# Kernel tuning notes

Measured on AMD Instinct MI355X. Metric: run time of the kernel, lower is better.

## Reference

```python
import jax, jax.numpy as jnp
import numpy as np

N_NODES = 100000
N_EDGES = 1200000
N_GRAPHS = 100  # hardcoded batch_size=100 in the original module


def gcn_conv(x, src, dst, W, b, n):
    """PyG GCNConv: x' = D^{-1/2} (A+I) D^{-1/2} (x W) + b, with self-loops appended."""
    x = x @ W  # [n, out]
    loop = jnp.arange(n, dtype=src.dtype)
    s = jnp.concatenate([src, loop])
    d = jnp.concatenate([dst, loop])
    deg = jax.ops.segment_sum(jnp.ones_like(d, dtype=x.dtype), d, num_segments=n)
    dinv = jax.lax.rsqrt(deg)  # deg >= 1 because of self-loops
    norm = dinv[s] * dinv[d]  # [E+n]
    out = jax.ops.segment_sum(x[s] * norm[:, None], d, num_segments=n)
    return out + b


def setup_inputs() -> dict:
    key = jax.random.key(0)
    ks = jax.random.split(key, 20)
    x = jax.random.normal(ks[0], (N_NODES, 5), dtype=jnp.float32)
    edge_index = jax.random.randint(ks[1], (2, N_EDGES), 0, N_NODES, dtype=jnp.int64)
    batch = jnp.sort(jax.random.randint(ks[2], (N_NODES,), 0, N_GRAPHS, dtype=jnp.int64))

    def lin(k, i, o):
        kw, kb = jax.random.split(k)
        W = jax.random.normal(kw, (i, o), dtype=jnp.float32) * (1.0 / np.sqrt(i))
        b = jax.random.normal(kb, (o,), dtype=jnp.float32) * 0.01
        return W, b

    W1, b1 = lin(ks[3], 5, 32)
    W2, b2 = lin(ks[4], 32, 64)
    nn1_W, nn1_b = lin(ks[5], 64, 124)
    nn2_W, nn2_b = lin(ks[6], 124 * 4, 64)
    W4, b4 = lin(ks[7], 64, 32)
    nn3_W, nn3_b = lin(ks[8], 32, 16)
    nn4_W, nn4_b = lin(ks[9], 16, 1)
    return {
        "x": x, "edge_index": edge_index, "batch": batch,
        "W1": W1, "b1": b1, "W2": W2, "b2": b2,
        "nn1_W": nn1_W, "nn1_b": nn1_b, "nn2_W": nn2_W, "nn2_b": nn2_b,
        "W4": W4, "b4": b4, "nn3_W": nn3_W, "nn3_b": nn3_b,
        "nn4_W": nn4_W, "nn4_b": nn4_b,
    }


def reference(x, edge_index, batch, W1, b1, W2, b2, nn1_W, nn1_b, nn2_W, nn2_b,
              W4, b4, nn3_W, nn3_b, nn4_W, nn4_b):
    src, dst = edge_index[0], edge_index[1]
    h = jax.nn.relu(gcn_conv(x, src, dst, W1, b1, N_NODES))
    h = jax.nn.relu(gcn_conv(h, src, dst, W2, b2, N_NODES))
    h = h @ nn1_W + nn1_b  # [N, 124]

    # four-way scatter pooling over graph ids
    cnt = jax.ops.segment_sum(jnp.ones((N_NODES,), h.dtype), batch, num_segments=N_GRAPHS)
    nonempty = (cnt > 0)[:, None]
    a = jax.ops.segment_max(h, batch, num_segments=N_GRAPHS)
    a = jnp.where(nonempty, a, 0.0)
    b_ = jax.ops.segment_min(h, batch, num_segments=N_GRAPHS)
    b_ = jnp.where(nonempty, b_, 0.0)
    c = jax.ops.segment_sum(h, batch, num_segments=N_GRAPHS)
    d = c / jnp.maximum(cnt, 1.0)[:, None]

    g = jax.nn.relu(jnp.concatenate([a, b_, c, d], axis=1))  # [100, 496]
    g = g @ nn2_W + nn2_b  # [100, 64]

    # conv4 over self-loop-only edge_index on the 100 pooled graph nodes
    loop = jnp.arange(N_GRAPHS)
    g = jax.nn.relu(gcn_conv(g, loop, loop, W4, b4, N_GRAPHS))
    g = jax.nn.relu(g @ nn3_W + nn3_b)
    return g @ nn4_W + nn4_b  # [100, 1]
```

## Files before the change

### kernel.cpp

```cpp
#include <hip/hip_runtime.h>
#include <hip/hip_bf16.h>
#include <math.h>

#define N_NODES  100000
#define N_EDGES  1200000
#define N_GRAPHS 100
#define SCAN_B   1024
#define XRNG     ((N_NODES + 7) / 8)
#define PARTS    16

__global__ void k_degslot(const int* __restrict__ dst, int* __restrict__ deg,
                          int* __restrict__ slotpos, int e) {
    int i = blockIdx.x * blockDim.x + threadIdx.x;
    if (i < e) slotpos[i] = atomicAdd(&deg[dst[i]], 1);
}

__global__ __launch_bounds__(256) void k_fill_x(
    const int* __restrict__ src, const int* __restrict__ dst,
    const int* __restrict__ slotpos, const int* __restrict__ row_ptr,
    int* __restrict__ csr_src, int e, int nchunk) {
    int r = blockIdx.x & 7;
    int chunk = blockIdx.x >> 3;
    int lo = r * XRNG;
    int per = (e + nchunk - 1) / nchunk;
    int beg = chunk * per;
    int end = beg + per < e ? beg + per : e;
    for (int i = beg + threadIdx.x; i < end; i += 256) {
        int d = dst[i];
        if ((unsigned)(d - lo) < (unsigned)XRNG)
            csr_src[row_ptr[d] + slotpos[i]] = src[i];
    }
}

__global__ void k_block_sums(const int* __restrict__ deg, int* __restrict__ bsum, int n) {
    int i = blockIdx.x * SCAN_B + threadIdx.x;
    int v = (i < n) ? deg[i] : 0;
    #pragma unroll
    for (int d = 32; d > 0; d >>= 1) v += __shfl_xor(v, d);
    __shared__ int wsum[SCAN_B / 64];
    int lane = threadIdx.x & 63, w = threadIdx.x >> 6;
    if (lane == 0) wsum[w] = v;
    __syncthreads();
    if (threadIdx.x == 0) {
        int s = 0;
        #pragma unroll
        for (int k = 0; k < SCAN_B / 64; k++) s += wsum[k];
        bsum[blockIdx.x] = s;
    }
}

__global__ void k_scan_bsums(int* __restrict__ bsum, int nb) {
    __shared__ int s[256];
    int t = threadIdx.x;
    int v = (t < nb) ? bsum[t] : 0;
    s[t] = v;
    __syncthreads();
    for (int d = 1; d < 256; d <<= 1) {
        int u = (t >= d) ? s[t - d] : 0;
        __syncthreads();
        s[t] += u;
        __syncthreads();
    }
    if (t < nb) bsum[t] = s[t] - v;
}

__global__ void k_scan_final(const int* __restrict__ deg, const int* __restrict__ bsum,
                             const float* __restrict__ x,
                             int* __restrict__ row_ptr, float* __restrict__ dinv,
                             float* __restrict__ y0, int n, int n_edges) {
    int b = blockIdx.x;
    int i = b * SCAN_B + threadIdx.x;
    int v = (i < n) ? deg[i] : 0;
    int lane = threadIdx.x & 63, w = threadIdx.x >> 6;
    int inc = v;
    #pragma unroll
    for (int d = 1; d < 64; d <<= 1) {
        int u = __shfl_up(inc, d);
        if (lane >= d) inc += u;
    }
    __shared__ int wsum[SCAN_B / 64];
    __shared__ int woff[SCAN_B / 64];
    if (lane == 63) wsum[w] = inc;
    __syncthreads();
    if (threadIdx.x == 0) {
        int s = 0;
        #pragma unroll
        for (int k = 0; k < SCAN_B / 64; k++) { woff[k] = s; s += wsum[k]; }
    }
    __syncthreads();
    int excl = bsum[b] + woff[w] + (inc - v);
    if (i < n) {
        row_ptr[i] = excl;
        float di = rsqrtf((float)(v + 1));
        dinv[i] = di;
        float4 q0, q1;
        q0.x = x[i * 5 + 0] * di;
        q0.y = x[i * 5 + 1] * di;
        q0.z = x[i * 5 + 2] * di;
        q0.w = x[i * 5 + 3] * di;
        q1.x = x[i * 5 + 4] * di;
        q1.y = 0.f; q1.z = 0.f; q1.w = 0.f;
        *(float4*)&y0[(size_t)i * 8]     = q0;
        *(float4*)&y0[(size_t)i * 8 + 4] = q1;
    }
    if (b == 0 && threadIdx.x == 0) row_ptr[n] = n_edges;
}

__global__ __launch_bounds__(256) void k_agg1(
    const int* __restrict__ row_ptr, const int* __restrict__ csr_src,
    const float* __restrict__ y0, const float* __restrict__ dinv,
    const float* __restrict__ W1, const float* __restrict__ b1,
    float* __restrict__ y1, int n) {
    int wave = (blockIdx.x * blockDim.x + threadIdx.x) >> 6;
    if (wave >= n) return;
    int lane = threadIdx.x & 63;
    int f = lane & 7, ec = lane >> 3;
    int start = row_ptr[wave], end = row_ptr[wave + 1];
    float acc = 0.f;
    for (int e = start + ec; e < end; e += 8) {
        int s = csr_src[e];
        acc += y0[(size_t)s * 8 + f];
    }
    if (ec == 0) acc += y0[(size_t)wave * 8 + f];
    acc += __shfl_down(acc, 32);
    acc += __shfl_down(acc, 16);
    acc += __shfl_down(acc, 8);
    float di = dinv[wave];
    float s0[5];
    #pragma unroll
    for (int k = 0; k < 5; k++) s0[k] = __shfl(acc, k) * di;
    int fo = lane & 31;
    float hv = b1[fo];
    #pragma unroll
    for (int k = 0; k < 5; k++) hv += s0[k] * W1[k * 32 + fo];
    hv = hv > 0.f ? hv : 0.f;
    if (lane < 32) y1[(size_t)wave * 32 + lane] = hv * di;
}

__global__ __launch_bounds__(256) void k_agg2g(
    const int* __restrict__ row_ptr, const int* __restrict__ csr_src,
    const float* __restrict__ y1, const float* __restrict__ dinv,
    float* __restrict__ sv, int n) {
    int wave = (blockIdx.x * blockDim.x + threadIdx.x) >> 6;
    if (wave >= n) return;
    int lane = threadIdx.x & 63;
    int ec = lane >> 3, fq = lane & 7;
    int start = row_ptr[wave], end = row_ptr[wave + 1];
    float4 a0 = make_float4(0.f, 0.f, 0.f, 0.f);
    float4 a1 = make_float4(0.f, 0.f, 0.f, 0.f);
    int e = start + ec;
    for (; e + 8 < end; e += 16) {
        int s0 = csr_src[e], s1 = csr_src[e + 8];
        float4 v0 = *(const float4*)&y1[(size_t)s0 * 32 + fq * 4];
        float4 v1 = *(const float4*)&y1[(size_t)s1 * 32 + fq * 4];
        a0.x += v0.x; a0.y += v0.y; a0.z += v0.z; a0.w += v0.w;
        a1.x += v1.x; a1.y += v1.y; a1.z += v1.z; a1.w += v1.w;
    }
    for (; e < end; e += 8) {
        int s0 = csr_src[e];
        float4 v0 = *(const float4*)&y1[(size_t)s0 * 32 + fq * 4];
        a0.x += v0.x; a0.y += v0.y; a0.z += v0.z; a0.w += v0.w;
    }
    a0.x += a1.x; a0.y += a1.y; a0.z += a1.z; a0.w += a1.w;
    if (ec == 0) {
        float4 sl = *(const float4*)&y1[(size_t)wave * 32 + fq * 4];
        a0.x += sl.x; a0.y += sl.y; a0.z += sl.z; a0.w += sl.w;
    }
    a0.x += __shfl_down(a0.x, 32); a0.y += __shfl_down(a0.y, 32);
    a0.z += __shfl_down(a0.z, 32); a0.w += __shfl_down(a0.w, 32);
    a0.x += __shfl_down(a0.x, 16); a0.y += __shfl_down(a0.y, 16);
    a0.z += __shfl_down(a0.z, 16); a0.w += __shfl_down(a0.w, 16);
    a0.x += __shfl_down(a0.x, 8);  a0.y += __shfl_down(a0.y, 8);
    a0.z += __shfl_down(a0.z, 8);  a0.w += __shfl_down(a0.w, 8);
    if (lane < 8) {
        float di = dinv[wave];
        float4 r;
        r.x = a0.x * di; r.y = a0.y * di; r.z = a0.z * di; r.w = a0.w * di;
        *(float4*)&sv[(size_t)wave * 32 + fq * 4] = r;
    }
}

#define LTS 68
__global__ __launch_bounds__(256) void k_l2mm(
    const float* __restrict__ sv, const float* __restrict__ W2,
    const float* __restrict__ b2, const float* __restrict__ nn1W,
    const float* __restrict__ nn1b, float* __restrict__ h, int n) {
    __shared__ float lsW2[32 * 64];
    __shared__ float lsN[64 * 128];
    __shared__ float lsT[64 * LTS];

    int tid = threadIdx.x;
    int nb = blockIdx.x * 64;

    #pragma unroll
    for (int i = 0; i < 8; i++) lsW2[tid + i * 256] = W2[tid + i * 256];
    for (int idx = tid; idx < 64 * 124; idx += 256)
        lsN[(idx / 124) * 128 + (idx % 124)] = nn1W[idx];
    if (tid < 256) lsN[(tid >> 2) * 128 + 124 + (tid & 3)] = 0.f;
    {
        int node = tid >> 2, kq = (tid & 3) * 8;
        float4 v0, v1;
        if (nb + node < n) {
            v0 = *(const float4*)&sv[(size_t)(nb + node) * 32 + kq];
            v1 = *(const float4*)&sv[(size_t)(nb + node) * 32 + kq + 4];
        } else {
            v0 = make_float4(0.f, 0.f, 0.f, 0.f); v1 = v0;
        }
        lsT[(kq + 0) * LTS + node] = v0.x;
        lsT[(kq + 1) * LTS + node] = v0.y;
        lsT[(kq + 2) * LTS + node] = v0.z;
        lsT[(kq + 3) * LTS + node] = v0.w;
        lsT[(kq + 4) * LTS + node] = v1.x;
        lsT[(kq + 5) * LTS + node] = v1.y;
        lsT[(kq + 6) * LTS + node] = v1.z;
        lsT[(kq + 7) * LTS + node] = v1.w;
    }
    __syncthreads();

    int tf = tid & 15;
    int tn = tid >> 4;

    float c1[4][4] = {};
    #pragma unroll 4
    for (int k = 0; k < 32; k++) {
        float4 a = *(const float4*)&lsT[k * LTS + tn * 4];
        float4 w = *(const float4*)&lsW2[k * 64 + tf * 4];
        const float av[4] = {a.x, a.y, a.z, a.w};
        const float wv[4] = {w.x, w.y, w.z, w.w};
        #pragma unroll
        for (int i = 0; i < 4; i++)
            #pragma unroll
            for (int j = 0; j < 4; j++) c1[i][j] += av[i] * wv[j];
    }
    __syncthreads();
    {
        float4 bb = *(const float4*)&b2[tf * 4];
        const float bv[4] = {bb.x, bb.y, bb.z, bb.w};
        #pragma unroll
        for (int j = 0; j < 4; j++) {
            float4 col;
            col.x = fmaxf(c1[0][j] + bv[j], 0.f);
            col.y = fmaxf(c1[1][j] + bv[j], 0.f);
            col.z = fmaxf(c1[2][j] + bv[j], 0.f);
            col.w = fmaxf(c1[3][j] + bv[j], 0.f);
            *(float4*)&lsT[(tf * 4 + j) * LTS + tn * 4] = col;
        }
    }
    __syncthreads();

    float c2a[4][4] = {}, c2b[4][4] = {};
    #pragma unroll 2
    for (int k = 0; k < 64; k++) {
        float4 a  = *(const float4*)&lsT[k * LTS + tn * 4];
        float4 w1 = *(const float4*)&lsN[k * 128 + tf * 4];
        float4 w2 = *(const float4*)&lsN[k * 128 + 64 + tf * 4];
        const float av[4] = {a.x, a.y, a.z, a.w};
        const float w1v[4] = {w1.x, w1.y, w1.z, w1.w};
        const float w2v[4] = {w2.x, w2.y, w2.z, w2.w};
        #pragma unroll
        for (int i = 0; i < 4; i++)
            #pragma unroll
            for (int j = 0; j < 4; j++) {
                c2a[i][j] += av[i] * w1v[j];
                c2b[i][j] += av[i] * w2v[j];
            }
    }
    {
        float4 ba = *(const float4*)&nn1b[tf * 4];
        const float bav[4] = {ba.x, ba.y, ba.z, ba.w};
        float bbv[4] = {0.f, 0.f, 0.f, 0.f};
        if (tf < 15) {
            float4 bb = *(const float4*)&nn1b[64 + tf * 4];
            bbv[0] = bb.x; bbv[1] = bb.y; bbv[2] = bb.z; bbv[3] = bb.w;
        }
        #pragma unroll
        for (int i = 0; i < 4; i++) {
            int node = nb + tn * 4 + i;
            if (node >= n) break;
            float4 oa, ob;
            oa.x = c2a[i][0] + bav[0]; oa.y = c2a[i][1] + bav[1];
            oa.z = c2a[i][2] + bav[2]; oa.w = c2a[i][3] + bav[3];
            *(float4*)&h[(size_t)node * 124 + tf * 4] = oa;
            if (tf < 15) {
                ob.x = c2b[i][0] + bbv[0]; ob.y = c2b[i][1] + bbv[1];
                ob.z = c2b[i][2] + bbv[2]; ob.w = c2b[i][3] + bbv[3];
                *(float4*)&h[(size_t)node * 124 + 64 + tf * 4] = ob;
            }
        }
    }
}

__global__ __launch_bounds__(512) void k_pool_a(
    const float* __restrict__ h, const int* __restrict__ batch,
    float* __restrict__ pmax, float* __restrict__ pmin, float* __restrict__ psum,
    int n) {
    int g = blockIdx.x / PARTS, r = blockIdx.x % PARTS;
    __shared__ int sb[2];
    if (threadIdx.x < 2) {
        int target = g + threadIdx.x;
        int lo = 0, hi = n;
        while (lo < hi) {
            int mid = (lo + hi) >> 1;
            if (batch[mid] < target) lo = mid + 1; else hi = mid;
        }
        sb[threadIdx.x] = lo;
    }
    __syncthreads();
    int start = sb[0], end = sb[1];
    int t = threadIdx.x;
    int f = t & 127, r2 = t >> 7;
    float vmax = -INFINITY, vmin = INFINITY, vsum = 0.f;
    if (f < 124) {
        for (int node = start + r * 4 + r2; node < end; node += PARTS * 4) {
            float v = h[(size_t)node * 124 + f];
            vmax = fmaxf(vmax, v);
            vmin = fminf(vmin, v);
            vsum += v;
        }
    }
    __shared__ float smax[4][128], smin[4][128], ssum[4][128];
    smax[r2][f] = vmax; smin[r2][f] = vmin; ssum[r2][f] = vsum;
    __syncthreads();
    if (r2 == 0) {
        #pragma unroll
        for (int k = 1; k < 4; k++) {
            vmax = fmaxf(vmax, smax[k][f]);
            vmin = fminf(vmin, smin[k][f]);
            vsum += ssum[k][f];
        }
        int idx = (g * PARTS + r) * 128 + f;
        pmax[idx] = vmax; pmin[idx] = vmin; psum[idx] = vsum;
    }
}

__global__ __launch_bounds__(256) void k_head(
    const float* __restrict__ pmax, const float* __restrict__ pmin,
    const float* __restrict__ psum, const int* __restrict__ batch,
    const float* __restrict__ nn2W, const float* __restrict__ nn2b,
    const float* __restrict__ W4,   const float* __restrict__ b4,
    const float* __restrict__ nn3W, const float* __restrict__ nn3b,
    const float* __restrict__ nn4W, const float* __restrict__ nn4b,
    float* __restrict__ out, int n) {
    int g = blockIdx.x, tid = threadIdx.x;
    int lane = tid & 63, w = tid >> 6;
    __shared__ float lg[496];
    __shared__ float part[4][64];
    __shared__ int sb[2];
    if (tid < 2) {
        int target = g + tid;
        int lo = 0, hi = n;
        while (lo < hi) {
            int mid = (lo + hi) >> 1;
            if (batch[mid] < target) lo = mid + 1; else hi = mid;
        }
        sb[tid] = lo;
    }
    __syncthreads();
    if (tid < 124) {
        float vmax = -INFINITY, vmin = INFINITY, vsum = 0.f;
        #pragma unroll 4
        for (int r = 0; r < PARTS; r++) {
            int idx = (g * PARTS + r) * 128 + tid;
            vmax = fmaxf(vmax, pmax[idx]);
            vmin = fminf(vmin, pmin[idx]);
            vsum += psum[idx];
        }
        int cnt = sb[1] - sb[0];
        float a = (cnt > 0) ? vmax : 0.f;
        float b = (cnt > 0) ? vmin : 0.f;
        lg[tid]       = fmaxf(a, 0.f);
        lg[124 + tid] = fmaxf(b, 0.f);
        lg[248 + tid] = fmaxf(vsum, 0.f);
        lg[372 + tid] = fmaxf(vsum / fmaxf((float)cnt, 1.f), 0.f);
    }
    __syncthreads();
    float acc = 0.f;
    int k0 = w * 124;
    #pragma unroll 4
    for (int k = k0; k < k0 + 124; k++)
        acc += lg[k] * nn2W[k * 64 + lane];
    part[w][lane] = acc;
    __syncthreads();
    if (w == 0) {
        float g1 = part[0][lane] + part[1][lane] + part[2][lane] + part[3][lane]
                 + nn2b[lane];
        float acc2 = (lane < 32) ? b4[lane] : 0.f;
        #pragma unroll 8
        for (int k = 0; k < 64; k++) {
            float v = __shfl(g1, k);
            if (lane < 32) acc2 += v * W4[k * 32 + lane];
        }
        float g2 = fmaxf(acc2, 0.f);
        float acc3 = (lane < 16) ? nn3b[lane] : 0.f;
        #pragma unroll 8
        for (int k = 0; k < 32; k++) {
            float v = __shfl(g2, k);
            if (lane < 16) acc3 += v * nn3W[k * 16 + lane];
        }
        float g3 = fmaxf(acc3, 0.f);
        float p = (lane < 16) ? g3 * nn4W[lane] : 0.f;
        p += __shfl_xor(p, 8);
        p += __shfl_xor(p, 4);
        p += __shfl_xor(p, 2);
        p += __shfl_xor(p, 1);
        if (lane == 0) out[g] = p + nn4b[0];
    }
}

extern "C" void kernel_launch(void* const* d_in, const int* in_sizes, int n_in,
                              void* d_out, int out_size, void* d_ws, size_t ws_size,
                              hipStream_t stream) {
    const int N = N_NODES, E = N_EDGES, G = N_GRAPHS;

    const float* x     = (const float*)d_in[0];
    const int*   ei    = (const int*)d_in[1];
    const int*   batch = (const int*)d_in[2];
    const float* W1    = (const float*)d_in[3];
    const float* b1    = (const float*)d_in[4];
    const float* W2    = (const float*)d_in[5];
    const float* b2    = (const float*)d_in[6];
    const float* nn1W  = (const float*)d_in[7];
    const float* nn1b  = (const float*)d_in[8];
    const float* nn2W  = (const float*)d_in[9];
    const float* nn2b  = (const float*)d_in[10];
    const float* W4    = (const float*)d_in[11];
    const float* b4    = (const float*)d_in[12];
    const float* nn3W  = (const float*)d_in[13];
    const float* nn3b  = (const float*)d_in[14];
    const float* nn4W  = (const float*)d_in[15];
    const float* nn4b  = (const float*)d_in[16];

    const int* src = ei;
    const int* dst = ei + E;

    char* ws = (char*)d_ws;
    size_t off = 0;
    auto alloc = [&](size_t bytes) -> char* {
        char* p = ws + off;
        off += (bytes + 255) & ~(size_t)255;
        return p;
    };
    int*   deg     = (int*)  alloc((size_t)N * 4);
    float* dinv    = (float*)alloc((size_t)N * 4);
    int*   row_ptr = (int*)  alloc((size_t)(N + 1) * 4);
    int*   slotpos = (int*)  alloc((size_t)E * 4);
    int*   bsum    = (int*)  alloc(1024 * 4);
    int*   csr_src = (int*)  alloc((size_t)E * 4);
    float* y0      = (float*)alloc((size_t)N * 8 * 4);
    float* y1      = (float*)alloc((size_t)N * 32 * 4);
    float* sv      = (float*)alloc((size_t)N * 32 * 4);
    float* h       = (float*)alloc((size_t)N * 124 * 4);
    float* pmax    = (float*)alloc((size_t)G * PARTS * 128 * 4);
    float* pmin    = (float*)alloc((size_t)G * PARTS * 128 * 4);
    float* psum    = (float*)alloc((size_t)G * PARTS * 128 * 4);
    (void)ws_size;

    float* out = (float*)d_out;

    const int NB = (N + SCAN_B - 1) / SCAN_B;
    const int NCHUNK = 256;

    hipMemsetAsync(deg, 0, (size_t)N * 4, stream);
    k_degslot<<<(E + 255) / 256, 256, 0, stream>>>(dst, deg, slotpos, E);
    k_block_sums<<<NB, SCAN_B, 0, stream>>>(deg, bsum, N);
    k_scan_bsums<<<1, 256, 0, stream>>>(bsum, NB);
    k_scan_final<<<NB, SCAN_B, 0, stream>>>(deg, bsum, x, row_ptr, dinv, y0, N, E);
    k_fill_x<<<NCHUNK * 8, 256, 0, stream>>>(src, dst, slotpos, row_ptr, csr_src, E, NCHUNK);
    k_agg1<<<(N + 3) / 4, 256, 0, stream>>>(row_ptr, csr_src, y0, dinv, W1, b1, y1, N);
    k_agg2g<<<(N + 3) / 4, 256, 0, stream>>>(row_ptr, csr_src, y1, dinv, sv, N);
    k_l2mm<<<(N + 63) / 64, 256, 0, stream>>>(sv, W2, b2, nn1W, nn1b, h, N);
    k_pool_a<<<G * PARTS, 512, 0, stream>>>(h, batch, pmax, pmin, psum, N);
    k_head<<<G, 256, 0, stream>>>(pmax, pmin, psum, batch, nn2W, nn2b, W4, b4,
                                  nn3W, nn3b, nn4W, nn4b, out, N);
}
```

Measured before the change: 346.4 us.

## Build CSR via two-level bucket sort with shared-memory histograms instead of global atomics

Replaces CSR construction, which used global atomic degree counting, a three-kernel scan and a filtered scatter, with a two-pass bucketed counting sort. Nodes are grouped into 512-node buckets. Per-block shared-memory histograms and a global bucket offset scan let (dst,src) pairs be scattered into contiguous bucket ranges. A per-bucket kernel then builds row_ptr, dinv, y0 and csr_src locally. This removes the 1.2M contended global atomics and the random slotpos traffic, at the cost of an extra 8-byte pair buffer pass.

```diff
diff --git a/kernel.cpp b/kernel.cpp
--- a/kernel.cpp
+++ b/kernel.cpp
@@ -5,105 +5,143 @@
 #define N_NODES  100000
 #define N_EDGES  1200000
 #define N_GRAPHS 100
-#define SCAN_B   1024
-#define XRNG     ((N_NODES + 7) / 8)
+#define NPB      512
+#define NBK      196
+#define BA       256
 #define PARTS    16
 
-__global__ void k_degslot(const int* __restrict__ dst, int* __restrict__ deg,
-                          int* __restrict__ slotpos, int e) {
-    int i = blockIdx.x * blockDim.x + threadIdx.x;
-    if (i < e) slotpos[i] = atomicAdd(&deg[dst[i]], 1);
-}
-
-__global__ __launch_bounds__(256) void k_fill_x(
+__global__ __launch_bounds__(1024) void k_hist(
+    const int* __restrict__ dst, int* __restrict__ hcnt, int e) {
+    __shared__ int hist[NBK];
+    int blk = blockIdx.x;
+    for (int j = threadIdx.x; j < NBK; j += 1024) hist[j] = 0;
+    __syncthreads();
+    int per = (e + BA - 1) / BA;
+    int beg = blk * per;
+    int end = beg + per < e ? beg + per : e;
+    for (int i = beg + threadIdx.x; i < end; i += 1024)
+        atomicAdd(&hist[dst[i] >> 9], 1);
+    __syncthreads();
+    for (int j = threadIdx.x; j < NBK; j += 1024) hcnt[blk * NBK + j] = hist[j];
+}
+
+__global__ __launch_bounds__(256) void k_bstart(
+    const int* __restrict__ hcnt, int* __restrict__ bstart,
+    int* __restrict__ row_ptr, int e) {
+    int b = threadIdx.x;
+    int s = 0;
+    if (b < NBK) {
+        #pragma unroll 8
+        for (int blk = 0; blk < BA; blk++) s += hcnt[blk * NBK + b];
+    }
+    __shared__ int sc[256];
+    sc[b] = s;
+    __syncthreads();
+    for (int d = 1; d < 256; d <<= 1) {
+        int u = (b >= d) ? sc[b - d] : 0;
+        __syncthreads();
+        sc[b] += u;
+        __syncthreads();
+    }
+    if (b < NBK) bstart[b] = sc[b] - s;
+    if (b == 0) { bstart[NBK] = e; row_ptr[N_NODES] = e; }
+}
+
+__global__ __launch_bounds__(256) void k_bdist(
+    int* __restrict__ hcnt, const int* __restrict__ bstart) {
+    int b = blockIdx.x, t = threadIdx.x;
+    int v = hcnt[t * NBK + b];
+    __shared__ int sc[256];
+    sc[t] = v;
+    __syncthreads();
+    for (int d = 1; d < 256; d <<= 1) {
+        int u = (t >= d) ? sc[t - d] : 0;
+        __syncthreads();
+        sc[t] += u;
+        __syncthreads();
+    }
+    hcnt[t * NBK + b] = bstart[b] + (sc[t] - v);
+}
+
+__global__ __launch_bounds__(1024) void k_scatter(
     const int* __restrict__ src, const int* __restrict__ dst,
-    const int* __restrict__ slotpos, const int* __restrict__ row_ptr,
-    int* __restrict__ csr_src, int e, int nchunk) {
-    int r = blockIdx.x & 7;
-    int chunk = blockIdx.x >> 3;
-    int lo = r * XRNG;
-    int per = (e + nchunk - 1) / nchunk;
-    int beg = chunk * per;
+    const int* __restrict__ hcnt, int2* __restrict__ pairs, int e) {
+    __shared__ int lbase[NBK];
+    __shared__ int cnt[NBK];
+    int blk = blockIdx.x;
+    for (int j = threadIdx.x; j < NBK; j += 1024) {
+        lbase[j] = hcnt[blk * NBK + j];
+        cnt[j] = 0;
+    }
+    __syncthreads();
+    int per = (e + BA - 1) / BA;
+    int beg = blk * per;
     int end = beg + per < e ? beg + per : e;
-    for (int i = beg + threadIdx.x; i < end; i += 256) {
-        int d = dst[i];
-        if ((unsigned)(d - lo) < (unsigned)XRNG)
-            csr_src[row_ptr[d] + slotpos[i]] = src[i];
-    }
-}
-
-__global__ void k_block_sums(const int* __restrict__ deg, int* __restrict__ bsum, int n) {
-    int i = blockIdx.x * SCAN_B + threadIdx.x;
-    int v = (i < n) ? deg[i] : 0;
-    #pragma unroll
-    for (int d = 32; d > 0; d >>= 1) v += __shfl_xor(v, d);
-    __shared__ int wsum[SCAN_B / 64];
-    int lane = threadIdx.x & 63, w = threadIdx.x >> 6;
-    if (lane == 0) wsum[w] = v;
-    __syncthreads();
-    if (threadIdx.x == 0) {
-        int s = 0;
-        #pragma unroll
-        for (int k = 0; k < SCAN_B / 64; k++) s += wsum[k];
-        bsum[blockIdx.x] = s;
-    }
-}
-
-__global__ void k_scan_bsums(int* __restrict__ bsum, int nb) {
-    __shared__ int s[256];
-    int t = threadIdx.x;
-    int v = (t < nb) ? bsum[t] : 0;
-    s[t] = v;
-    __syncthreads();
-    for (int d = 1; d < 256; d <<= 1) {
-        int u = (t >= d) ? s[t - d] : 0;
-        __syncthreads();
-        s[t] += u;
-        __syncthreads();
-    }
-    if (t < nb) bsum[t] = s[t] - v;
-}
-
-__global__ void k_scan_final(const int* __restrict__ deg, const int* __restrict__ bsum,
-                             const float* __restrict__ x,
-                             int* __restrict__ row_ptr, float* __restrict__ dinv,
-                             float* __restrict__ y0, int n, int n_edges) {
-    int b = blockIdx.x;
-    int i = b * SCAN_B + threadIdx.x;
-    int v = (i < n) ? deg[i] : 0;
-    int lane = threadIdx.x & 63, w = threadIdx.x >> 6;
+    for (int i = beg + threadIdx.x; i < end; i += 1024) {
+        int d = dst[i], s = src[i];
+        int b = d >> 9;
+        int r = atomicAdd(&cnt[b], 1);
+        pairs[lbase[b] + r] = make_int2(d, s);
+    }
+}
+
+__global__ __launch_bounds__(512) void k_bucket(
+    const int2* __restrict__ pairs, const int* __restrict__ bstart,
+    const float* __restrict__ x,
+    int* __restrict__ row_ptr, float* __restrict__ dinv,
+    float* __restrict__ y0, int* __restrict__ csr_src, int n) {
+    __shared__ int hist[NPB];
+    __shared__ int labs[NPB];
+    __shared__ int wsum[8], woff[8];
+    int b = blockIdx.x, t = threadIdx.x;
+    int beg = bstart[b], end = bstart[b + 1];
+    hist[t] = 0;
+    __syncthreads();
+    for (int i = beg + t; i < end; i += 512)
+        atomicAdd(&hist[pairs[i].x & (NPB - 1)], 1);
+    __syncthreads();
+    int v = hist[t];
+    int lane = t & 63, w = t >> 6;
     int inc = v;
     #pragma unroll
     for (int d = 1; d < 64; d <<= 1) {
         int u = __shfl_up(inc, d);
         if (lane >= d) inc += u;
     }
-    __shared__ int wsum[SCAN_B / 64];
-    __shared__ int woff[SCAN_B / 64];
     if (lane == 63) wsum[w] = inc;
     __syncthreads();
-    if (threadIdx.x == 0) {
+    if (t == 0) {
         int s = 0;
         #pragma unroll
-        for (int k = 0; k < SCAN_B / 64; k++) { woff[k] = s; s += wsum[k]; }
-    }
-    __syncthreads();
-    int excl = bsum[b] + woff[w] + (inc - v);
-    if (i < n) {
-        row_ptr[i] = excl;
+        for (int k = 0; k < 8; k++) { woff[k] = s; s += wsum[k]; }
+    }
+    __syncthreads();
+    int excl = woff[w] + inc - v;
+    labs[t] = beg + excl;
+    int node = (b << 9) + t;
+    if (node < n) {
+        row_ptr[node] = beg + excl;
         float di = rsqrtf((float)(v + 1));
-        dinv[i] = di;
+        dinv[node] = di;
         float4 q0, q1;
-        q0.x = x[i * 5 + 0] * di;
-        q0.y = x[i * 5 + 1] * di;
-        q0.z = x[i * 5 + 2] * di;
-        q0.w = x[i * 5 + 3] * di;
-        q1.x = x[i * 5 + 4] * di;
+        q0.x = x[(size_t)node * 5 + 0] * di;
+        q0.y = x[(size_t)node * 5 + 1] * di;
+        q0.z = x[(size_t)node * 5 + 2] * di;
+        q0.w = x[(size_t)node * 5 + 3] * di;
+        q1.x = x[(size_t)node * 5 + 4] * di;
         q1.y = 0.f; q1.z = 0.f; q1.w = 0.f;
-        *(float4*)&y0[(size_t)i * 8]     = q0;
-        *(float4*)&y0[(size_t)i * 8 + 4] = q1;
-    }
-    if (b == 0 && threadIdx.x == 0) row_ptr[n] = n_edges;
+        *(float4*)&y0[(size_t)node * 8]     = q0;
+        *(float4*)&y0[(size_t)node * 8 + 4] = q1;
+    }
+    __syncthreads();
+    hist[t] = 0;
+    __syncthreads();
+    for (int i = beg + t; i < end; i += 512) {
+        int2 p = pairs[i];
+        int j = p.x & (NPB - 1);
+        int r = atomicAdd(&hist[j], 1);
+        csr_src[labs[j] + r] = p.y;
+    }
 }
 
 __global__ __launch_bounds__(256) void k_agg1(
@@ -440,11 +478,11 @@
         off += (bytes + 255) & ~(size_t)255;
         return p;
     };
-    int*   deg     = (int*)  alloc((size_t)N * 4);
+    int*   hcnt    = (int*)  alloc((size_t)BA * NBK * 4);
+    int*   bstart  = (int*)  alloc((NBK + 1) * 4);
+    int2*  pairs   = (int2*) alloc((size_t)E * 8);
+    int*   row_ptr = (int*)  alloc((size_t)(N + 1) * 4);
     float* dinv    = (float*)alloc((size_t)N * 4);
-    int*   row_ptr = (int*)  alloc((size_t)(N + 1) * 4);
-    int*   slotpos = (int*)  alloc((size_t)E * 4);
-    int*   bsum    = (int*)  alloc(1024 * 4);
     int*   csr_src = (int*)  alloc((size_t)E * 4);
     float* y0      = (float*)alloc((size_t)N * 8 * 4);
     float* y1      = (float*)alloc((size_t)N * 32 * 4);
@@ -457,15 +495,11 @@
 
     float* out = (float*)d_out;
 
-    const int NB = (N + SCAN_B - 1) / SCAN_B;
-    const int NCHUNK = 256;
-
-    hipMemsetAsync(deg, 0, (size_t)N * 4, stream);
-    k_degslot<<<(E + 255) / 256, 256, 0, stream>>>(dst, deg, slotpos, E);
-    k_block_sums<<<NB, SCAN_B, 0, stream>>>(deg, bsum, N);
-    k_scan_bsums<<<1, 256, 0, stream>>>(bsum, NB);
-    k_scan_final<<<NB, SCAN_B, 0, stream>>>(deg, bsum, x, row_ptr, dinv, y0, N, E);
-    k_fill_x<<<NCHUNK * 8, 256, 0, stream>>>(src, dst, slotpos, row_ptr, csr_src, E, NCHUNK);
+    k_hist<<<BA, 1024, 0, stream>>>(dst, hcnt, E);
+    k_bstart<<<1, 256, 0, stream>>>(hcnt, bstart, row_ptr, E);
+    k_bdist<<<NBK, 256, 0, stream>>>(hcnt, bstart);
+    k_scatter<<<BA, 1024, 0, stream>>>(src, dst, hcnt, pairs, E);
+    k_bucket<<<NBK, 512, 0, stream>>>(pairs, bstart, x, row_ptr, dinv, y0, csr_src, N);
     k_agg1<<<(N + 3) / 4, 256, 0, stream>>>(row_ptr, csr_src, y0, dinv, W1, b1, y1, N);
     k_agg2g<<<(N + 3) / 4, 256, 0, stream>>>(row_ptr, csr_src, y1, dinv, sv, N);
     k_l2mm<<<(N + 63) / 64, 256, 0, stream>>>(sv, W2, b2, nn1W, nn1b, h, N);
```

Measured after the change: 301.5 us. -12.9%, faster.
